# Kernel tuning notes

Hardware: AMD Instinct MI355X
Metric: run time of the kernel (lower is better)

Reference implementation:

```python
import jax, jax.numpy as jnp
import numpy as np

B, L, S, H, E, D = 2, 2048, 2048, 16, 64, 64

def setup_inputs() -> dict:
    key = jax.random.key(0)
    kq, kk, kv = jax.random.split(key, 3)
    queries = jax.random.normal(kq, (B, L, H, E), dtype=jnp.float32)
    keys = jax.random.normal(kk, (B, S, H, E), dtype=jnp.float32)
    values = jax.random.normal(kv, (B, S, H, D), dtype=jnp.float32)
    mask = jnp.zeros((1, 1, L, S), dtype=jnp.float32)  # additive mask, broadcast over B,H
    return {"queries": queries, "keys": keys, "values": values, "mask": mask}

def reference(queries, keys, values, mask):
    # scale defaults to 1/sqrt(E)
    scale = 1.0 / jnp.sqrt(jnp.asarray(queries.shape[-1], queries.dtype))
    # scores: [B,H,L,S]
    scores = jnp.einsum('blhe,bshe->bhls', queries, keys)
    scores = scores + mask
    A = jax.nn.softmax(scale * scores, axis=-1)  # dropout rate 0 => identity
    V = jnp.einsum('bhls,bshd->blhd', A, values)
    return V
```

## Files before the change

kernel.cpp:

```cpp
#include <hip/hip_runtime.h>
#include <stdint.h>

typedef _Float16 half8 __attribute__((ext_vector_type(8)));
typedef _Float16 half4 __attribute__((ext_vector_type(4)));
typedef float f32x4 __attribute__((ext_vector_type(4)));

constexpr int B = 2, L = 2048, S = 2048, H = 16, E = 64, D = 64;
constexpr int BM = 128;
constexpr int BN = 64;
constexpr int NTI = S / BN;
constexpr float CS = 0.125f * 1.44269504089f;

constexpr size_t KH_HALFS = (size_t)B * H * S * E;
constexpr size_t VT_HALFS = (size_t)B * H * D * S;
constexpr size_t MH_HALFS = (size_t)L * S;
constexpr size_t WS_NEED  = (KH_HALFS + VT_HALFS + MH_HALFS) * 2;

__global__ __launch_bounds__(256, 4)
void prep_kernel(const float* __restrict__ Kg, const float* __restrict__ Vg,
                 const float* __restrict__ Mg, _Float16* __restrict__ ws)
{
    _Float16* Kh  = ws;
    _Float16* VTh = ws + KH_HALFS;
    _Float16* Mh  = ws + KH_HALFS + VT_HALFS;
    const int tid = threadIdx.x;
    const int bid = blockIdx.x;

    if (bid < 2048) {
        const int idx = bid * 256 + tid;
        const int c   = idx & 7;
        const int s   = (idx >> 3) & 2047;
        const int bh  = idx >> 14;
        const int b   = bh >> 4, h = bh & 15;
        const float* src = Kg + ((size_t)(b * S + s)) * (H * E) + h * E + c * 8;
        const float4 v0 = *(const float4*)(src);
        const float4 v1 = *(const float4*)(src + 4);
        half8 o = {(_Float16)v0.x, (_Float16)v0.y, (_Float16)v0.z, (_Float16)v0.w,
                   (_Float16)v1.x, (_Float16)v1.y, (_Float16)v1.z, (_Float16)v1.w};
        *(half8*)(Kh + (((size_t)bh * S + s) << 6) + ((c ^ (s & 7)) * 8)) = o;
    } else if (bid < 4096) {
        const size_t idx = (size_t)(bid - 2048) * 256 + tid;
        const float* src = Mg + idx * 8;
        const float4 v0 = *(const float4*)(src);
        const float4 v1 = *(const float4*)(src + 4);
        half8 o = {(_Float16)(v0.x*CS), (_Float16)(v0.y*CS), (_Float16)(v0.z*CS),
                   (_Float16)(v0.w*CS), (_Float16)(v1.x*CS), (_Float16)(v1.y*CS),
                   (_Float16)(v1.z*CS), (_Float16)(v1.w*CS)};
        *(half8*)(Mh + idx * 8) = o;
    } else {
        __shared__ _Float16 tile[64][72];
        const int bid2 = bid - 4096;
        const int sblk = bid2 & 31;
        const int h    = (bid2 >> 5) & 15;
        const int b    = bid2 >> 9;
        const int ts = tid >> 4, d4 = (tid & 15) << 2;
        #pragma unroll
        for (int ii = 0; ii < 4; ++ii) {
            const int sl = ts + ii * 16;
            const float4 v = *(const float4*)(Vg + ((size_t)(b * S + sblk*64 + sl)) * (H * D) + h * D + d4);
            #pragma unroll
            for (int j = 0; j < 4; ++j)
                tile[d4 + j][sl] = (_Float16)((&v.x)[j]);
        }
        __syncthreads();
        const int d = tid >> 2, cp = tid & 3;
        _Float16* drow = VTh + (((size_t)(b * H + h) * D + d) << 11) + sblk * 64;
        #pragma unroll
        for (int k = 0; k < 2; ++k) {
            const int chunk = cp * 2 + k;
            half8 o;
            #pragma unroll
            for (int j = 0; j < 8; ++j) o[j] = tile[d][chunk * 8 + j];
            *(half8*)(drow + ((chunk ^ (d & 7)) * 8)) = o;
        }
    }
}

__device__ __forceinline__ void gload16(const _Float16* g, const _Float16* l) {
    __builtin_amdgcn_global_load_lds(
        (const __attribute__((address_space(1))) uint32_t*)(uintptr_t)(g),
        (__attribute__((address_space(3))) uint32_t*)(uintptr_t)(l),
        16, 0, 0);
}

#define STAGE(BUF, S0)                                                          \
{                                                                               \
    _Pragma("unroll")                                                           \
    for (int ii = 0; ii < 2; ++ii) {                                            \
        const int r = wave * 16 + ii * 8;                                       \
        gload16(kh_bh + ((size_t)((S0) + r + (lane >> 3)) << 6) + (lane & 7)*8, \
                &sK[BUF][r][0]);                                                \
        gload16(vt_bh + ((size_t)(r + (lane >> 3)) << 11) + (S0) + (lane & 7)*8,\
                &sV[BUF][r][0]);                                                \
    }                                                                           \
}

#define TILE_STEP(BUF, MC, MN, T)                                                           \
{                                                                                           \
    if ((T) + 1 < NTI) STAGE((BUF) ^ 1, ((T) + 1) * BN)                                     \
                       \
    f32x4 sf[2][4];                                                                         \
    __builtin_amdgcn_s_setprio(1);                                                          \
    _Pragma("unroll")                                                                       \
    for (int nt = 0; nt < 4; ++nt) {                                                        \
        half8 kf0 = *(const half8*)&sK[BUF][nt*16 + lq][((    quad) ^ (lq & 7)) * 8];       \
        half8 kf1 = *(const half8*)&sK[BUF][nt*16 + lq][((4 + quad) ^ (lq & 7)) * 8];       \
        _Pragma("unroll")                                                                   \
        for (int g = 0; g < 2; ++g) {                                                       \
            f32x4 acc = (f32x4){0.f, 0.f, 0.f, 0.f};                                        \
            acc = __builtin_amdgcn_mfma_f32_16x16x32_f16(kf0, qf[g][0], acc, 0, 0, 0);      \
            acc = __builtin_amdgcn_mfma_f32_16x16x32_f16(kf1, qf[g][1], acc, 0, 0, 0);      \
            sf[g][nt] = acc;                                                                \
        }                                                                                   \
    }                                                                                       \
    __builtin_amdgcn_s_setprio(0);                                                          \
                               \
    _Pragma("unroll")                                                                       \
    for (int g = 0; g < 2; ++g) {                                                           \
        _Float16* prow = &sP[wave][g*16 + lq][0];                                           \
        _Pragma("unroll")                                                                   \
        for (int nt = 0; nt < 4; ++nt) {                                                    \
            half4 hp;                                                                       \
            _Pragma("unroll")                                                               \
            for (int r = 0; r < 4; ++r) {                                                   \
                float lg = sf[g][nt][r] + (float)MC[g*4 + nt][r];                           \
                float p  = __builtin_amdgcn_exp2f(lg);                                      \
                lsum[g] += p;                                                               \
                hp[r] = (_Float16)p;                                                        \
            }                                                                               \
            *(half4*)(prow + (((2*nt + (quad >> 1)) ^ (lq & 7)) * 8 + (quad & 1) * 4)) = hp;\
        }                                                                                   \
    }                                                                                       \
                          \
    if ((T) + 1 < NTI) {                                                                    \
        const int s1_ = ((T) + 1) * BN;                                                     \
        _Pragma("unroll")                                                                   \
        for (int g = 0; g < 2; ++g)                                                         \
            _Pragma("unroll")                                                               \
            for (int nt = 0; nt < 4; ++nt)                                                  \
                MN[g*4 + nt] = *(const half4*)(mrow0 + ((size_t)g << 15)                    \
                                               + s1_ + nt*16 + quad*4);                     \
    }                                                                                       \
                                                        \
    __builtin_amdgcn_s_setprio(1);                                                          \
    _Pragma("unroll")                                                                       \
    for (int ks = 0; ks < 2; ++ks) {                                                        \
        half8 pf0 = *(const half8*)&sP[wave][     lq][((4*ks + quad) ^ (lq & 7)) * 8];      \
        half8 pf1 = *(const half8*)&sP[wave][16 + lq][((4*ks + quad) ^ (lq & 7)) * 8];      \
        _Pragma("unroll")                                                                   \
        for (int dt = 0; dt < 4; ++dt) {                                                    \
            half8 vf = *(const half8*)&sV[BUF][dt*16 + lq][((4*ks + quad) ^ (lq & 7)) * 8]; \
            oacc[0][dt] = __builtin_amdgcn_mfma_f32_16x16x32_f16(pf0, vf, oacc[0][dt],0,0,0);\
            oacc[1][dt] = __builtin_amdgcn_mfma_f32_16x16x32_f16(pf1, vf, oacc[1][dt],0,0,0);\
        }                                                                                   \
    }                                                                                       \
    __builtin_amdgcn_s_setprio(0);                                                          \
    if ((T) + 1 < NTI) __syncthreads();            \
}

__global__ __launch_bounds__(256, 2)
void fa3_kernel(const float* __restrict__ Qg, const _Float16* __restrict__ ws,
                float* __restrict__ Og)
{
    __shared__ _Float16 sK[2][BN][64];
    __shared__ _Float16 sV[2][D][64];
    __shared__ _Float16 sP[4][32][64];

    const _Float16* Kh  = ws;
    const _Float16* VTh = ws + KH_HALFS;
    const _Float16* Mh  = ws + KH_HALFS + VT_HALFS;

    const int tid  = threadIdx.x;
    const int wave = tid >> 6;
    const int lane = tid & 63;
    const int quad = lane >> 4;
    const int lq   = lane & 15;

    const int i  = blockIdx.x;
    const int bh = (i & 7) * 4 + ((i >> 3) & 3);
    const int qb = i >> 5;
    const int b  = bh >> 4;
    const int h  = bh & 15;
    const int q0 = qb * BM;

    const int rowStride = H * E;
    const size_t qbase = ((size_t)b * L) * rowStride + h * E;

    const _Float16* kh_bh = Kh  + ((size_t)(b * H + h) << 17);
    const _Float16* vt_bh = VTh + ((size_t)(b * H + h) << 17);
    const _Float16* mrow0 = Mh  + ((size_t)(q0 + wave * 32 + lq) << 11);

    half8 qf[2][2];
    #pragma unroll
    for (int g = 0; g < 2; ++g) {
        const float* qp = Qg + qbase + (size_t)(q0 + wave*32 + g*16 + lq) * rowStride + quad*8;
        #pragma unroll
        for (int ks = 0; ks < 2; ++ks)
            #pragma unroll
            for (int j = 0; j < 8; ++j)
                qf[g][ks][j] = (_Float16)(qp[ks*32 + j] * CS);
    }

    float lsum[2] = {0.f, 0.f};
    f32x4 oacc[2][4];
    #pragma unroll
    for (int g = 0; g < 2; ++g)
        #pragma unroll
        for (int dt = 0; dt < 4; ++dt) oacc[g][dt] = (f32x4){0.f, 0.f, 0.f, 0.f};

    half4 mA[8], mB[8];

    STAGE(0, 0)
    #pragma unroll
    for (int g = 0; g < 2; ++g)
        #pragma unroll
        for (int nt = 0; nt < 4; ++nt)
            mA[g*4 + nt] = *(const half4*)(mrow0 + ((size_t)g << 15) + nt*16 + quad*4);
    __syncthreads();

    for (int tt = 0; tt < NTI; tt += 2) {
        TILE_STEP(0, mA, mB, tt)
        TILE_STEP(1, mB, mA, tt + 1)
    }

    #pragma unroll
    for (int g = 0; g < 2; ++g) {
        float l = lsum[g];
        l += __shfl_xor(l, 16);
        l += __shfl_xor(l, 32);
        #pragma unroll
        for (int r = 0; r < 4; ++r) {
            float l_bc = __shfl(l, quad*4 + r, 16);
            float inv = 1.f / l_bc;
            float* orow = Og + qbase + (size_t)(q0 + wave*32 + g*16 + quad*4 + r) * rowStride;
            #pragma unroll
            for (int dt = 0; dt < 4; ++dt)
                orow[dt*16 + lq] = oacc[g][dt][r] * inv;
        }
    }
}

constexpr int LDT = 72;

__global__ __launch_bounds__(256, 2)
void fa_fb_kernel(const float* __restrict__ Qg, const float* __restrict__ Kg,
                  const float* __restrict__ Vg, const float* __restrict__ Mg,
                  float* __restrict__ Og)
{
    __shared__ _Float16 sK[BN][LDT];
    __shared__ _Float16 sV[D][LDT];
    __shared__ _Float16 sP[4][32][LDT];

    const int tid  = threadIdx.x;
    const int wave = tid >> 6;
    const int lane = tid & 63;
    const int quad = lane >> 4;
    const int lq   = lane & 15;

    const int i  = blockIdx.x;
    const int bh = (i & 7) * 4 + ((i >> 3) & 3);
    const int qb = i >> 5;
    const int b  = bh >> 4;
    const int h  = bh & 15;
    const int q0 = qb * BM;

    const int rowStride = H * E;
    const size_t qbase = ((size_t)b * L) * rowStride + h * E;
    const size_t kbase = ((size_t)b * S) * rowStride + h * E;

    half8 qf[2][2];
    #pragma unroll
    for (int g = 0; g < 2; ++g) {
        const float* qp = Qg + qbase + (size_t)(q0 + wave*32 + g*16 + lq) * rowStride + quad*8;
        #pragma unroll
        for (int ks = 0; ks < 2; ++ks)
            #pragma unroll
            for (int j = 0; j < 8; ++j)
                qf[g][ks][j] = (_Float16)(qp[ks*32 + j] * CS);
    }

    const float* mrow0 = Mg + (size_t)(q0 + wave*32 + lq) * S;

    float lsum[2] = {0.f, 0.f};
    f32x4 oacc[2][4];
    #pragma unroll
    for (int g = 0; g < 2; ++g)
        #pragma unroll
        for (int dt = 0; dt < 4; ++dt) oacc[g][dt] = (f32x4){0.f, 0.f, 0.f, 0.f};

    const int db = tid & 15;
    const int sb = tid >> 4;
    const float* vbase = Vg + kbase + (size_t)(sb*4) * rowStride + db*4;
    const float* krow  = Kg + kbase + (size_t)(tid >> 4) * rowStride + (tid & 15)*4;
    const int voff = (((sb >> 1) ^ (db >> 1)) << 3) + ((sb & 1) << 2);

    float4 kreg[4], vreg[4], mreg[2][4];

    #pragma unroll
    for (int ii = 0; ii < 4; ++ii)
        kreg[ii] = *(const float4*)(krow + (size_t)(ii*16) * rowStride);
    #pragma unroll
    for (int j = 0; j < 4; ++j)
        vreg[j] = *(const float4*)(vbase + (size_t)j * rowStride);
    #pragma unroll
    for (int g = 0; g < 2; ++g)
        #pragma unroll
        for (int nt = 0; nt < 4; ++nt)
            mreg[g][nt] = *(const float4*)(mrow0 + (size_t)g*16*S + nt*16 + quad*4);

    #pragma unroll
    for (int ii = 0; ii < 4; ++ii) {
        half4 hk = {(_Float16)kreg[ii].x, (_Float16)kreg[ii].y,
                    (_Float16)kreg[ii].z, (_Float16)kreg[ii].w};
        *(half4*)&sK[(tid >> 4) + ii*16][(tid & 15)*4] = hk;
    }
    #pragma unroll
    for (int j = 0; j < 4; ++j) {
        half4 hv = { (_Float16)((&vreg[0].x)[j]), (_Float16)((&vreg[1].x)[j]),
                     (_Float16)((&vreg[2].x)[j]), (_Float16)((&vreg[3].x)[j]) };
        *(half4*)&sV[db*4 + j][voff] = hv;
    }
    __syncthreads();

    for (int t = 0; t < NTI; ++t) {
        if (t + 1 < NTI) {
            const int s1 = (t + 1) * BN;
            #pragma unroll
            for (int ii = 0; ii < 4; ++ii)
                kreg[ii] = *(const float4*)(krow + (size_t)(s1 + ii*16) * rowStride);
            #pragma unroll
            for (int j = 0; j < 4; ++j)
                vreg[j] = *(const float4*)(vbase + (size_t)(s1 + j) * rowStride);
        }

        f32x4 sf[2][4];
        __builtin_amdgcn_s_setprio(1);
        #pragma unroll
        for (int nt = 0; nt < 4; ++nt) {
            half8 kf0 = *(const half8*)&sK[nt*16 + lq][ 0 + quad*8];
            half8 kf1 = *(const half8*)&sK[nt*16 + lq][32 + quad*8];
            #pragma unroll
            for (int g = 0; g < 2; ++g) {
                f32x4 acc = (f32x4){0.f, 0.f, 0.f, 0.f};
                acc = __builtin_amdgcn_mfma_f32_16x16x32_f16(kf0, qf[g][0], acc, 0, 0, 0);
                acc = __builtin_amdgcn_mfma_f32_16x16x32_f16(kf1, qf[g][1], acc, 0, 0, 0);
                sf[g][nt] = acc;
            }
        }
        __builtin_amdgcn_s_setprio(0);

        #pragma unroll
        for (int g = 0; g < 2; ++g)
            #pragma unroll
            for (int nt = 0; nt < 4; ++nt) {
                half4 hp;
                #pragma unroll
                for (int r = 0; r < 4; ++r) {
                    float lg = fmaf((&mreg[g][nt].x)[r], CS, sf[g][nt][r]);
                    float p  = __builtin_amdgcn_exp2f(lg);
                    lsum[g] += p;
                    hp[r] = (_Float16)p;
                }
                *(half4*)&sP[wave][g*16 + lq][nt*16 + quad*4] = hp;
            }

        if (t + 1 < NTI) {
            const int s1 = (t + 1) * BN;
            #pragma unroll
            for (int g = 0; g < 2; ++g)
                #pragma unroll
                for (int nt = 0; nt < 4; ++nt)
                    mreg[g][nt] = *(const float4*)(mrow0 + (size_t)g*16*S + s1 + nt*16 + quad*4);
        }

        __builtin_amdgcn_s_setprio(1);
        #pragma unroll
        for (int ks = 0; ks < 2; ++ks) {
            half8 pf0 = *(const half8*)&sP[wave][ 0 + lq][ks*32 + quad*8];
            half8 pf1 = *(const half8*)&sP[wave][16 + lq][ks*32 + quad*8];
            #pragma unroll
            for (int dt = 0; dt < 4; ++dt) {
                const int vrow = dt*16 + lq;
                const int phys = (ks*4 + quad) ^ ((vrow >> 3) & 7);
                half8 vf = *(const half8*)&sV[vrow][phys << 3];
                oacc[0][dt] = __builtin_amdgcn_mfma_f32_16x16x32_f16(pf0, vf, oacc[0][dt], 0, 0, 0);
                oacc[1][dt] = __builtin_amdgcn_mfma_f32_16x16x32_f16(pf1, vf, oacc[1][dt], 0, 0, 0);
            }
        }
        __builtin_amdgcn_s_setprio(0);

        if (t + 1 < NTI) {
            __syncthreads();
            #pragma unroll
            for (int ii = 0; ii < 4; ++ii) {
                half4 hk = {(_Float16)kreg[ii].x, (_Float16)kreg[ii].y,
                            (_Float16)kreg[ii].z, (_Float16)kreg[ii].w};
                *(half4*)&sK[(tid >> 4) + ii*16][(tid & 15)*4] = hk;
            }
            #pragma unroll
            for (int j = 0; j < 4; ++j) {
                half4 hv = { (_Float16)((&vreg[0].x)[j]), (_Float16)((&vreg[1].x)[j]),
                             (_Float16)((&vreg[2].x)[j]), (_Float16)((&vreg[3].x)[j]) };
                *(half4*)&sV[db*4 + j][voff] = hv;
            }
            __syncthreads();
        }
    }

    #pragma unroll
    for (int g = 0; g < 2; ++g) {
        float l = lsum[g];
        l += __shfl_xor(l, 16);
        l += __shfl_xor(l, 32);
        #pragma unroll
        for (int r = 0; r < 4; ++r) {
            float l_bc = __shfl(l, quad*4 + r, 16);
            float inv = 1.f / l_bc;
            float* orow = Og + qbase + (size_t)(q0 + wave*32 + g*16 + quad*4 + r) * rowStride;
            #pragma unroll
            for (int dt = 0; dt < 4; ++dt)
                orow[dt*16 + lq] = oacc[g][dt][r] * inv;
        }
    }
}

extern "C" void kernel_launch(void* const* d_in, const int* in_sizes, int n_in,
                              void* d_out, int out_size, void* d_ws, size_t ws_size,
                              hipStream_t stream) {
    const float* Qg = (const float*)d_in[0];
    const float* Kg = (const float*)d_in[1];
    const float* Vg = (const float*)d_in[2];
    const float* Mg = (const float*)d_in[3];
    float* Og = (float*)d_out;

    if (ws_size >= WS_NEED && d_ws != nullptr) {
        _Float16* ws = (_Float16*)d_ws;
        prep_kernel<<<dim3(2048 + 2048 + 1024), 256, 0, stream>>>(Kg, Vg, Mg, ws);
        fa3_kernel<<<dim3((L / BM) * B * H), 256, 0, stream>>>(Qg, ws, Og);
    } else {
        fa_fb_kernel<<<dim3((L / BM) * B * H), 256, 0, stream>>>(Qg, Kg, Vg, Mg, Og);
    }
}
```

Measured before the change: 175.9 us.

## Stage 128-key K/V tiles per buffer and halve block-wide barriers

Each double-buffered LDS stage now holds 128 keys of K and V instead of 64. Every staged tile is consumed as two 64-key half-steps, so the main loop needs one __syncthreads per 128 keys rather than per 64. Async loads are issued at a coarser granularity. The cost is LDS use growing from about 48KB to 80KB per block, plus a wider 256-byte V row stride that may change bank-conflict behaviour.

```diff
diff --git a/kernel.cpp b/kernel.cpp
--- a/kernel.cpp
+++ b/kernel.cpp
@@ -8,7 +8,9 @@
 constexpr int B = 2, L = 2048, S = 2048, H = 16, E = 64, D = 64;
 constexpr int BM = 128;
 constexpr int BN = 64;
-constexpr int NTI = S / BN;
+constexpr int TN = 128;
+constexpr int NDT = S / TN;
+constexpr int NHS = S / BN;
 constexpr float CS = 0.125f * 1.44269504089f;
 
 constexpr size_t KH_HALFS = (size_t)B * H * S * E;
@@ -83,28 +85,31 @@
         16, 0, 0);
 }
 
-#define STAGE(BUF, S0)                                                          \
-{                                                                               \
-    _Pragma("unroll")                                                           \
-    for (int ii = 0; ii < 2; ++ii) {                                            \
-        const int r = wave * 16 + ii * 8;                                       \
-        gload16(kh_bh + ((size_t)((S0) + r + (lane >> 3)) << 6) + (lane & 7)*8, \
-                &sK[BUF][r][0]);                                                \
-        gload16(vt_bh + ((size_t)(r + (lane >> 3)) << 11) + (S0) + (lane & 7)*8,\
-                &sV[BUF][r][0]);                                                \
-    }                                                                           \
-}
-
-#define TILE_STEP(BUF, MC, MN, T)                                                           \
+#define STAGE(BUF, S0)                                                            \
+{                                                                                 \
+    _Pragma("unroll")                                                             \
+    for (int ii = 0; ii < 4; ++ii) {                                              \
+        const int kr = wave * 32 + ii * 8;                                        \
+        gload16(kh_bh + ((size_t)((S0) + kr + (lane >> 3)) << 6) + (lane & 7)*8,  \
+                &sK[BUF][kr][0]);                                                 \
+    }                                                                             \
+    _Pragma("unroll")                                                             \
+    for (int ii = 0; ii < 4; ++ii) {                                              \
+        const int dr = wave * 16 + ii * 4;                                        \
+        gload16(vt_bh + ((size_t)(dr + (lane >> 4)) << 11) + (S0) + (lane & 15)*8,\
+                &sV[BUF][dr][0]);                                                 \
+    }                                                                             \
+}
+
+#define HALF_STEP(BUF, HS, MC, MN, TH)                                                      \
 {                                                                                           \
-    if ((T) + 1 < NTI) STAGE((BUF) ^ 1, ((T) + 1) * BN)                                     \
                        \
     f32x4 sf[2][4];                                                                         \
     __builtin_amdgcn_s_setprio(1);                                                          \
     _Pragma("unroll")                                                                       \
     for (int nt = 0; nt < 4; ++nt) {                                                        \
-        half8 kf0 = *(const half8*)&sK[BUF][nt*16 + lq][((    quad) ^ (lq & 7)) * 8];       \
-        half8 kf1 = *(const half8*)&sK[BUF][nt*16 + lq][((4 + quad) ^ (lq & 7)) * 8];       \
+        half8 kf0 = *(const half8*)&sK[BUF][(HS)*64 + nt*16 + lq][((    quad) ^ (lq & 7)) * 8];\
+        half8 kf1 = *(const half8*)&sK[BUF][(HS)*64 + nt*16 + lq][((4 + quad) ^ (lq & 7)) * 8];\
         _Pragma("unroll")                                                                   \
         for (int g = 0; g < 2; ++g) {                                                       \
             f32x4 acc = (f32x4){0.f, 0.f, 0.f, 0.f};                                        \
@@ -114,7 +119,7 @@
         }                                                                                   \
     }                                                                                       \
     __builtin_amdgcn_s_setprio(0);                                                          \
-                               \
+                  \
     _Pragma("unroll")                                                                       \
     for (int g = 0; g < 2; ++g) {                                                           \
         _Float16* prow = &sP[wave][g*16 + lq][0];                                           \
@@ -131,9 +136,9 @@
             *(half4*)(prow + (((2*nt + (quad >> 1)) ^ (lq & 7)) * 8 + (quad & 1) * 4)) = hp;\
         }                                                                                   \
     }                                                                                       \
-                          \
-    if ((T) + 1 < NTI) {                                                                    \
-        const int s1_ = ((T) + 1) * BN;                                                     \
+                                     \
+    if ((TH) + 1 < NHS) {                                                                   \
+        const int s1_ = ((TH) + 1) * BN;                                                    \
         _Pragma("unroll")                                                                   \
         for (int g = 0; g < 2; ++g)                                                         \
             _Pragma("unroll")                                                               \
@@ -149,21 +154,20 @@
         half8 pf1 = *(const half8*)&sP[wave][16 + lq][((4*ks + quad) ^ (lq & 7)) * 8];      \
         _Pragma("unroll")                                                                   \
         for (int dt = 0; dt < 4; ++dt) {                                                    \
-            half8 vf = *(const half8*)&sV[BUF][dt*16 + lq][((4*ks + quad) ^ (lq & 7)) * 8]; \
+            half8 vf = *(const half8*)&sV[BUF][dt*16 + lq][(HS)*64 + ((4*ks + quad) ^ (lq & 7)) * 8];\
             oacc[0][dt] = __builtin_amdgcn_mfma_f32_16x16x32_f16(pf0, vf, oacc[0][dt],0,0,0);\
             oacc[1][dt] = __builtin_amdgcn_mfma_f32_16x16x32_f16(pf1, vf, oacc[1][dt],0,0,0);\
         }                                                                                   \
     }                                                                                       \
     __builtin_amdgcn_s_setprio(0);                                                          \
-    if ((T) + 1 < NTI) __syncthreads();            \
 }
 
 __global__ __launch_bounds__(256, 2)
-void fa3_kernel(const float* __restrict__ Qg, const _Float16* __restrict__ ws,
+void fa4_kernel(const float* __restrict__ Qg, const _Float16* __restrict__ ws,
                 float* __restrict__ Og)
 {
-    __shared__ _Float16 sK[2][BN][64];
-    __shared__ _Float16 sV[2][D][64];
+    __shared__ _Float16 sK[2][TN][64];
+    __shared__ _Float16 sV[2][D][TN];
     __shared__ _Float16 sP[4][32][64];
 
     const _Float16* Kh  = ws;
@@ -218,9 +222,15 @@
             mA[g*4 + nt] = *(const half4*)(mrow0 + ((size_t)g << 15) + nt*16 + quad*4);
     __syncthreads();
 
-    for (int tt = 0; tt < NTI; tt += 2) {
-        TILE_STEP(0, mA, mB, tt)
-        TILE_STEP(1, mB, mA, tt + 1)
+    for (int t2 = 0; t2 < NDT; t2 += 2) {
+        STAGE(1, (t2 + 1) * TN)
+        HALF_STEP(0, 0, mA, mB, 2*t2)
+        HALF_STEP(0, 1, mB, mA, 2*t2 + 1)
+        __syncthreads();
+        if (t2 + 2 < NDT) STAGE(0, (t2 + 2) * TN)
+        HALF_STEP(1, 0, mA, mB, 2*t2 + 2)
+        HALF_STEP(1, 1, mB, mA, 2*t2 + 3)
+        if (t2 + 2 < NDT) __syncthreads();
     }
 
     #pragma unroll
@@ -322,8 +332,8 @@
     }
     __syncthreads();
 
-    for (int t = 0; t < NTI; ++t) {
-        if (t + 1 < NTI) {
+    for (int t = 0; t < NHS; ++t) {
+        if (t + 1 < NHS) {
             const int s1 = (t + 1) * BN;
             #pragma unroll
             for (int ii = 0; ii < 4; ++ii)
@@ -364,7 +374,7 @@
                 *(half4*)&sP[wave][g*16 + lq][nt*16 + quad*4] = hp;
             }
 
-        if (t + 1 < NTI) {
+        if (t + 1 < NHS) {
             const int s1 = (t + 1) * BN;
             #pragma unroll
             for (int g = 0; g < 2; ++g)
@@ -389,7 +399,7 @@
         }
         __builtin_amdgcn_s_setprio(0);
 
-        if (t + 1 < NTI) {
+        if (t + 1 < NHS) {
             __syncthreads();
             #pragma unroll
             for (int ii = 0; ii < 4; ++ii) {
@@ -436,7 +446,7 @@
     if (ws_size >= WS_NEED && d_ws != nullptr) {
         _Float16* ws = (_Float16*)d_ws;
         prep_kernel<<<dim3(2048 + 2048 + 1024), 256, 0, stream>>>(Kg, Vg, Mg, ws);
-        fa3_kernel<<<dim3((L / BM) * B * H), 256, 0, stream>>>(Qg, ws, Og);
+        fa4_kernel<<<dim3((L / BM) * B * H), 256, 0, stream>>>(Qg, ws, Og);
     } else {
         fa_fb_kernel<<<dim3((L / BM) * B * H), 256, 0, stream>>>(Qg, Kg, Vg, Mg, Og);
     }
```

Measured after the change: 196.6 us. 1.12x slower.
